# Performance work log

Measured on AMD Instinct MI355X. Metric: run time of the kernel, lower is better.

The kernel has to match this reference:

```python
import jax, jax.numpy as jnp
import numpy as np
from jax import lax

B, C, H, W = 8, 128, 128, 128
HEADS = 16
HEAD_C = C // HEADS  # 8
SLOPE = 0.2
EPS = 1e-12


def _conv(x, w, b, padding, groups=1):
    # x: [B,C,H,W], w: [O,I/groups,kh,kw]
    y = lax.conv_general_dilated(
        x, w, window_strides=(1, 1), padding=padding,
        dimension_numbers=("NCHW", "OIHW", "NCHW"),
        feature_group_count=groups)
    return y + b[None, :, None, None]


def _conv_block(x, conv1_w, conv1_b, conv2_w, conv2_b, dw_w, dw_b, sc_w, sc_b):
    h = _conv(x, conv1_w, conv1_b, ((1, 1), (1, 1)))            # 3x3, zero pad
    h = jnp.where(h >= 0, h, SLOPE * h)                          # LeakyReLU
    h = _conv(h, conv2_w, conv2_b, ((0, 0), (0, 0)))             # 1x1
    hp = jnp.pad(h, ((0, 0), (0, 0), (1, 1), (1, 1)), mode="reflect")
    h = _conv(hp, dw_w, dw_b, ((0, 0), (0, 0)), groups=C)        # depthwise 3x3, reflect pad
    h = jnp.where(h >= 0, h, SLOPE * h)
    sc = _conv(x, sc_w, sc_b, ((0, 0), (0, 0)))                  # 1x1 shortcut
    return h + sc


def setup_inputs() -> dict:
    key = jax.random.key(0)
    ks = jax.random.split(key, 10)
    s = 0.05
    return {
        "x1": jax.random.normal(ks[0], (B, C, H, W), jnp.float32),
        "x2": jax.random.normal(ks[1], (B, C, H, W), jnp.float32),
        "temperature": jnp.ones((HEADS, 1, 1), jnp.float32),
        "conv1_w": jax.random.normal(ks[2], (C, C, 3, 3), jnp.float32) * s,
        "conv1_b": jnp.zeros((C,), jnp.float32),
        "conv2_w": jax.random.normal(ks[3], (C, C, 1, 1), jnp.float32) * s,
        "conv2_b": jnp.zeros((C,), jnp.float32),
        "dw_w": jax.random.normal(ks[4], (C, 1, 3, 3), jnp.float32) * s,
        "dw_b": jnp.zeros((C,), jnp.float32),
        "sc_w": jax.random.normal(ks[5], (C, C, 1, 1), jnp.float32) * s,
        "sc_b": jnp.zeros((C,), jnp.float32),
    }


def reference(x1, x2, temperature, conv1_w, conv1_b, conv2_w, conv2_b,
              dw_w, dw_b, sc_w, sc_b):
    b, c, h, w = x2.shape
    # b (head c) h w -> b head c (h w)
    qk = x1.reshape(b, HEADS, HEAD_C, h * w)
    v = x2.reshape(b, HEADS, HEAD_C, h * w)
    # L2-normalize over spatial dim (F.normalize, eps=1e-12)
    norm = jnp.sqrt(jnp.sum(qk * qk, axis=-1, keepdims=True))
    qn = qk / jnp.maximum(norm, EPS)
    # channel attention: [b, head, c, c]
    attn = jnp.einsum("bhcn,bhdn->bhcd", qn, qn) * temperature
    attn = jax.nn.softmax(attn, axis=-1)
    out = jnp.einsum("bhcd,bhdn->bhcn", attn, v)
    out = out.reshape(b, c, h, w)
    out = _conv_block(out, conv1_w, conv1_b, conv2_w, conv2_b,
                      dw_w, dw_b, sc_w, sc_b)
    return out + x1
```

## Files before the change

kernel.cpp:

```cpp
#include <hip/hip_runtime.h>
#include <hip/hip_bf16.h>

typedef __attribute__((ext_vector_type(8))) short short8;
typedef __attribute__((ext_vector_type(4))) float f32x4;

#define NB 8
#define NC 128
#define NHW 128
#define NSP (NHW*NHW)
#define SLOPE 0.2f
#define EPSN 1e-12f

static __device__ __forceinline__ unsigned short f2bf(float f) {
    __hip_bfloat16 h = __float2bfloat16(f);
    return *reinterpret_cast<unsigned short*>(&h);
}
static __device__ __forceinline__ float bf2f(__hip_bfloat16 h) {
    return __bfloat162float(h);
}

__global__ void prep_wb1(const float* __restrict__ w, __hip_bfloat16* __restrict__ wb) {
    int idx = blockIdx.x * 256 + threadIdx.x;
    if (idx >= 128 * 128 * 9) return;
    int kw = idx % 3; int t = idx / 3;
    int kh = t % 3;   t /= 3;
    int i  = t % 128; int o = t / 128;
    int tap = kh * 3 + kw;
    int half = i >> 6, icc = (i >> 5) & 1, lk = (i >> 3) & 3, j = i & 7;
    int wn = o >> 6, c = (o >> 4) & 3, l15 = o & 15;
    int lane = lk * 16 + l15;
    size_t chunk = (size_t)tap * 32 + half * 16 + wn * 8 + icc * 4 + c;
    wb[chunk * 512 + lane * 8 + j] = __float2bfloat16(w[idx]);
}

__global__ void prep_w1x1(const float* __restrict__ w, __hip_bfloat16* __restrict__ wb) {
    int idx = blockIdx.x * 256 + threadIdx.x;
    if (idx >= 128 * 128) return;
    int i = idx & 127, o = idx >> 7;
    int kk = i >> 5, lk = (i >> 3) & 3, j = i & 7;
    int wn = o >> 6, c = (o >> 4) & 3, l15 = o & 15;
    int lane = lk * 16 + l15;
    size_t chunk = ((size_t)(wn * 4 + kk) * 4 + c);
    wb[chunk * 512 + lane * 8 + j] = __float2bfloat16(w[idx]);
}

__global__ __launch_bounds__(256) void gram_part(const float* __restrict__ x1,
                                                 float* __restrict__ Gp) {
    int bh = blockIdx.x & 127;
    int q  = blockIdx.x >> 7;
    const float* base = x1 + (size_t)bh * 8 * NSP + q * 4096;
    float acc[8][8];
#pragma unroll
    for (int c = 0; c < 8; c++)
#pragma unroll
        for (int d = 0; d < 8; d++) acc[c][d] = 0.f;

    for (int n = threadIdx.x; n < 4096; n += 256) {
        float v[8];
#pragma unroll
        for (int c = 0; c < 8; c++) v[c] = base[c * NSP + n];
#pragma unroll
        for (int c = 0; c < 8; c++)
#pragma unroll
            for (int d = 0; d < 8; d++)
                acc[c][d] = fmaf(v[c], v[d], acc[c][d]);
    }
#pragma unroll
    for (int c = 0; c < 8; c++)
#pragma unroll
        for (int d = 0; d < 8; d++)
            for (int off = 32; off > 0; off >>= 1)
                acc[c][d] += __shfl_down(acc[c][d], off);

    __shared__ float red[4][64];
    int wv = threadIdx.x >> 6;
    if ((threadIdx.x & 63) == 0) {
#pragma unroll
        for (int c = 0; c < 8; c++)
#pragma unroll
            for (int d = 0; d < 8; d++) red[wv][c * 8 + d] = acc[c][d];
    }
    __syncthreads();
    if (threadIdx.x < 64)
        Gp[(size_t)(q * 128 + bh) * 64 + threadIdx.x] =
            red[0][threadIdx.x] + red[1][threadIdx.x] + red[2][threadIdx.x] + red[3][threadIdx.x];
}

__global__ void gram_reduce(const float* __restrict__ Gp, float* __restrict__ G) {
    int bh = blockIdx.x;
    int t = threadIdx.x;
    float s = 0.f;
#pragma unroll
    for (int q = 0; q < 4; q++) s += Gp[(size_t)(q * 128 + bh) * 64 + t];
    G[bh * 64 + t] = s;
}

__global__ void softmax_kernel(const float* __restrict__ G, const float* __restrict__ temp,
                               float* __restrict__ attn) {
    int bh = blockIdx.x; int h = bh & 15;
    int t = threadIdx.x;
    int c = t >> 3, d = t & 7;
    const float* g = G + bh * 64;
    float nc = fmaxf(sqrtf(g[c * 8 + c]), EPSN);
    float nd = fmaxf(sqrtf(g[d * 8 + d]), EPSN);
    float a = g[t] / (nc * nd) * temp[h];
    float m = a;
#pragma unroll
    for (int off = 4; off > 0; off >>= 1) m = fmaxf(m, __shfl_xor(m, off));
    float e = __expf(a - m);
    float s = e;
#pragma unroll
    for (int off = 4; off > 0; off >>= 1) s += __shfl_xor(s, off);
    attn[bh * 64 + t] = e / s;
}

__global__ __launch_bounds__(256) void av_v2(const float* __restrict__ x2,
                                             const float* __restrict__ attn,
                                             __hip_bfloat16* __restrict__ yt) {
    int b  = blockIdx.x >> 8;
    int p0 = (blockIdx.x & 255) << 6;
    __shared__ float vt[128][65];
    __shared__ float at[16][65];
    for (int idx = threadIdx.x; idx < 1024; idx += 256)
        at[idx >> 6][idx & 63] = attn[(size_t)b * 1024 + idx];
    for (int idx = threadIdx.x; idx < 8192; idx += 256) {
        int row = idx >> 6, col = idx & 63;
        vt[row][col] = x2[(size_t)(b * 128 + row) * NSP + p0 + col];
    }
    __syncthreads();
    for (int idx = threadIdx.x; idx < 1024; idx += 256) {
        int cq = idx & 15;
        int p  = idx >> 4;
        float vv[8];
#pragma unroll
        for (int d = 0; d < 8; d++) vv[d] = vt[cq * 8 + d][p];
        unsigned int pk[4];
#pragma unroll
        for (int c = 0; c < 8; c += 2) {
            float s0 = 0.f, s1 = 0.f;
#pragma unroll
            for (int d = 0; d < 8; d++) {
                s0 = fmaf(at[cq][c * 8 + d], vv[d], s0);
                s1 = fmaf(at[cq][(c + 1) * 8 + d], vv[d], s1);
            }
            pk[c >> 1] = (unsigned int)f2bf(s0) | ((unsigned int)f2bf(s1) << 16);
        }
        uint4 st; st.x = pk[0]; st.y = pk[1]; st.z = pk[2]; st.w = pk[3];
        *reinterpret_cast<uint4*>(yt + ((size_t)b * NSP + p0 + p) * 128 + cq * 8) = st;
    }
}

__global__ __launch_bounds__(256, 4) void fused_conv(const __hip_bfloat16* __restrict__ yt,
                                                     const __hip_bfloat16* __restrict__ wb1,
                                                     const __hip_bfloat16* __restrict__ wb2,
                                                     const __hip_bfloat16* __restrict__ wbsc,
                                                     const float* __restrict__ b1,
                                                     const float* __restrict__ b2,
                                                     const float* __restrict__ bsc,
                                                     const float* __restrict__ x1,
                                                     __hip_bfloat16* __restrict__ h2,
                                                     float* __restrict__ out) {
    __shared__ uint4 smem[1584];
    char* smem_raw = (char*)smem;
    int bid = blockIdx.x;
    int swz = (bid & 7) * 256 + (bid >> 3);
    int b = swz >> 8;
    int rh = swz & 255;
    int h = rh >> 1;
    int p0 = (rh & 1) * 64;
    int tid = threadIdx.x;
    int lane = tid & 63;
    int wid = tid >> 6;
    int wm = wid >> 1, wn = wid & 1;
    int l15 = lane & 15;
    int lk = lane >> 4;

    const short8* wf1  = reinterpret_cast<const short8*>(wb1);
    const short8* wf2  = reinterpret_cast<const short8*>(wb2);
    const short8* wfsc = reinterpret_cast<const short8*>(wbsc);

    f32x4 acc[2][4];
#pragma unroll
    for (int a = 0; a < 2; a++)
#pragma unroll
        for (int c = 0; c < 4; c++) acc[a][c] = (f32x4){0.f, 0.f, 0.f, 0.f};

#pragma unroll
    for (int half = 0; half < 2; ++half) {
        __syncthreads();
        for (int idx = tid; idx < 1584; idx += 256) {
            int g = idx & 7;
            int colr = idx >> 3;
            int col = colr % 66;
            int r = colr / 66;
            int hh = h + r - 1;
            int w = p0 + col - 1;
            uint4 v = make_uint4(0u, 0u, 0u, 0u);
            if ((unsigned)hh < 128u && (unsigned)w < 128u)
                v = *reinterpret_cast<const uint4*>(
                    yt + (((size_t)(b * 128 + hh)) * 128 + w) * 128 + half * 64 + g * 8);
            smem[(r * 66 + col) * 8 + (g ^ (col & 7))] = v;
        }
        __syncthreads();

        int cgrp = half * 16 + wn * 8;
        const short8* wp0 = wf1 + (size_t)cgrp * 64 + lane;
        short8 cb0 = wp0[0], cb1 = wp0[64], cb2 = wp0[128], cb3 = wp0[192];

#pragma unroll
        for (int gi = 0; gi < 18; ++gi) {
            int tap = gi >> 1, icc = gi & 1;
            int kh = tap / 3, kw = tap - kh * 3;
            short8 nb0, nb1, nb2, nb3;
            if (gi < 17) {
                int gin = gi + 1;
                const short8* wpn = wf1 +
                    (size_t)(((gin >> 1) * 32) + cgrp + (gin & 1) * 4) * 64 + lane;
                nb0 = wpn[0]; nb1 = wpn[64]; nb2 = wpn[128]; nb3 = wpn[192];
            }
            short8 afr[2];
#pragma unroll
            for (int a = 0; a < 2; ++a) {
                int col = (wm * 2 + a) * 16 + l15 + kw;
                int g = icc * 4 + lk;
                afr[a] = *reinterpret_cast<const short8*>(
                    &smem[(kh * 66 + col) * 8 + (g ^ (col & 7))]);
            }
            __builtin_amdgcn_s_setprio(1);
#pragma unroll
            for (int a = 0; a < 2; ++a) {
                acc[a][0] = __builtin_amdgcn_mfma_f32_16x16x32_bf16(afr[a], cb0, acc[a][0], 0, 0, 0);
                acc[a][1] = __builtin_amdgcn_mfma_f32_16x16x32_bf16(afr[a], cb1, acc[a][1], 0, 0, 0);
                acc[a][2] = __builtin_amdgcn_mfma_f32_16x16x32_bf16(afr[a], cb2, acc[a][2], 0, 0, 0);
                acc[a][3] = __builtin_amdgcn_mfma_f32_16x16x32_bf16(afr[a], cb3, acc[a][3], 0, 0, 0);
            }
            __builtin_amdgcn_s_setprio(0);
            cb0 = nb0; cb1 = nb1; cb2 = nb2; cb3 = nb3;
        }
    }

    __syncthreads();
#pragma unroll
    for (int c = 0; c < 4; ++c) {
        int o = wn * 64 + c * 16 + l15;
        float bv = b1[o];
        int go = o >> 3, ob = (o & 7) << 1;
#pragma unroll
        for (int a = 0; a < 2; ++a) {
            int pb = (wm * 2 + a) * 16 + lk * 4;
#pragma unroll
            for (int j = 0; j < 4; ++j) {
                int p = pb + j;
                float v = acc[a][c][j] + bv;
                v = v >= 0.f ? v : SLOPE * v;
                *reinterpret_cast<__hip_bfloat16*>(
                    smem_raw + p * 256 + (((go ^ (p & 15)) << 4) | ob)) = __float2bfloat16(v);
            }
        }
    }
    __syncthreads();

#pragma unroll
    for (int a = 0; a < 2; a++)
#pragma unroll
        for (int c = 0; c < 4; c++) acc[a][c] = (f32x4){0.f, 0.f, 0.f, 0.f};
#pragma unroll
    for (int kk = 0; kk < 4; ++kk) {
        short8 bfr[4];
#pragma unroll
        for (int c = 0; c < 4; ++c)
            bfr[c] = wf2[((size_t)(wn * 4 + kk) * 4 + c) * 64 + lane];
        short8 afr[2];
        int g = kk * 4 + lk;
#pragma unroll
        for (int a = 0; a < 2; ++a) {
            int p = (wm * 2 + a) * 16 + l15;
            afr[a] = *reinterpret_cast<const short8*>(smem_raw + p * 256 + ((g ^ (p & 15)) << 4));
        }
        __builtin_amdgcn_s_setprio(1);
#pragma unroll
        for (int a = 0; a < 2; ++a)
#pragma unroll
            for (int c = 0; c < 4; ++c)
                acc[a][c] = __builtin_amdgcn_mfma_f32_16x16x32_bf16(afr[a], bfr[c], acc[a][c], 0, 0, 0);
        __builtin_amdgcn_s_setprio(0);
    }
#pragma unroll
    for (int c = 0; c < 4; ++c) {
        int o = wn * 64 + c * 16 + l15;
        float bv = b2[o];
        size_t obase = ((size_t)(b * 128 + o) * 128 + h) * 128 + p0;
#pragma unroll
        for (int a = 0; a < 2; ++a) {
            int w0 = (wm * 2 + a) * 16 + lk * 4;
            uint2 st;
            st.x = (unsigned int)f2bf(acc[a][c][0] + bv) | ((unsigned int)f2bf(acc[a][c][1] + bv) << 16);
            st.y = (unsigned int)f2bf(acc[a][c][2] + bv) | ((unsigned int)f2bf(acc[a][c][3] + bv) << 16);
            *reinterpret_cast<uint2*>(h2 + obase + w0) = st;
        }
    }

    __syncthreads();
    for (int idx = tid; idx < 1024; idx += 256) {
        int p = idx >> 4, g = idx & 15;
        uint4 v = *reinterpret_cast<const uint4*>(
            yt + ((size_t)(b * NSP + h * 128 + p0 + p)) * 128 + g * 8);
        *reinterpret_cast<uint4*>(smem_raw + p * 256 + ((g ^ (p & 15)) << 4)) = v;
    }
    __syncthreads();

#pragma unroll
    for (int a = 0; a < 2; a++)
#pragma unroll
        for (int c = 0; c < 4; c++) acc[a][c] = (f32x4){0.f, 0.f, 0.f, 0.f};
#pragma unroll
    for (int kk = 0; kk < 4; ++kk) {
        short8 bfr[4];
#pragma unroll
        for (int c = 0; c < 4; ++c)
            bfr[c] = wfsc[((size_t)(wn * 4 + kk) * 4 + c) * 64 + lane];
        short8 afr[2];
        int g = kk * 4 + lk;
#pragma unroll
        for (int a = 0; a < 2; ++a) {
            int p = (wm * 2 + a) * 16 + l15;
            afr[a] = *reinterpret_cast<const short8*>(smem_raw + p * 256 + ((g ^ (p & 15)) << 4));
        }
        __builtin_amdgcn_s_setprio(1);
#pragma unroll
        for (int a = 0; a < 2; ++a)
#pragma unroll
            for (int c = 0; c < 4; ++c)
                acc[a][c] = __builtin_amdgcn_mfma_f32_16x16x32_bf16(afr[a], bfr[c], acc[a][c], 0, 0, 0);
        __builtin_amdgcn_s_setprio(0);
    }
#pragma unroll
    for (int c = 0; c < 4; ++c) {
        int o = wn * 64 + c * 16 + l15;
        float bv = bsc[o];
        size_t obase = ((size_t)(b * 128 + o) * 128 + h) * 128 + p0;
#pragma unroll
        for (int a = 0; a < 2; ++a) {
            int w0 = (wm * 2 + a) * 16 + lk * 4;
            float4 xv = *reinterpret_cast<const float4*>(x1 + obase + w0);
            float4 st;
            st.x = acc[a][c][0] + bv + xv.x;
            st.y = acc[a][c][1] + bv + xv.y;
            st.z = acc[a][c][2] + bv + xv.z;
            st.w = acc[a][c][3] + bv + xv.w;
            *reinterpret_cast<float4*>(out + obase + w0) = st;
        }
    }
}

__global__ __launch_bounds__(256) void dw_v2(const __hip_bfloat16* __restrict__ h2,
                                             const float* __restrict__ dww,
                                             const float* __restrict__ dwb,
                                             float* __restrict__ out) {
    int bid = blockIdx.x;
    int swz = (bid & 7) * 1024 + (bid >> 3);
    size_t tidx = (size_t)swz * 256 + threadIdx.x;
    int w0 = (int)((tidx & 15) << 3);
    int hh = (int)((tidx >> 4) & 127);
    int bc = (int)(tidx >> 11);
    int c  = bc & 127;
    const __hip_bfloat16* src = h2 + ((size_t)bc << 14);
    float wg[9];
#pragma unroll
    for (int k = 0; k < 9; ++k) wg[k] = dww[c * 9 + k];
    float bv = dwb[c];
    float a8[8];
#pragma unroll
    for (int j = 0; j < 8; ++j) a8[j] = bv;
#pragma unroll
    for (int kh = 0; kh < 3; ++kh) {
        int ih = hh + kh - 1;
        ih = ih < 0 ? 1 : (ih > 127 ? 126 : ih);
        const __hip_bfloat16* row = src + ih * 128;
        short8 mid = *reinterpret_cast<const short8*>(row + w0);
        float v[10];
        v[0] = bf2f(row[w0 == 0 ? 1 : w0 - 1]);
#pragma unroll
        for (int j = 0; j < 8; ++j)
            v[j + 1] = __uint_as_float((unsigned int)(unsigned short)mid[j] << 16);
        v[9] = bf2f(row[w0 == 120 ? 126 : w0 + 8]);
#pragma unroll
        for (int kw = 0; kw < 3; ++kw)
#pragma unroll
            for (int j = 0; j < 8; ++j)
                a8[j] = fmaf(v[j + kw], wg[kh * 3 + kw], a8[j]);
    }
    size_t ob = ((size_t)bc << 14) + hh * 128 + w0;
    float4 o0 = *reinterpret_cast<const float4*>(out + ob);
    float4 o1 = *reinterpret_cast<const float4*>(out + ob + 4);
#pragma unroll
    for (int j = 0; j < 8; ++j) a8[j] = a8[j] >= 0.f ? a8[j] : SLOPE * a8[j];
    o0.x += a8[0]; o0.y += a8[1]; o0.z += a8[2]; o0.w += a8[3];
    o1.x += a8[4]; o1.y += a8[5]; o1.z += a8[6]; o1.w += a8[7];
    *reinterpret_cast<float4*>(out + ob) = o0;
    *reinterpret_cast<float4*>(out + ob + 4) = o1;
}

extern "C" void kernel_launch(void* const* d_in, const int* in_sizes, int n_in,
                              void* d_out, int out_size, void* d_ws, size_t ws_size,
                              hipStream_t stream) {
    const float* x1   = (const float*)d_in[0];
    const float* x2   = (const float*)d_in[1];
    const float* temp = (const float*)d_in[2];
    const float* c1w  = (const float*)d_in[3];
    const float* c1b  = (const float*)d_in[4];
    const float* c2w  = (const float*)d_in[5];
    const float* c2b  = (const float*)d_in[6];
    const float* dww  = (const float*)d_in[7];
    const float* dwb  = (const float*)d_in[8];
    const float* scw  = (const float*)d_in[9];
    const float* scb  = (const float*)d_in[10];
    float* out = (float*)d_out;
    char* ws = (char*)d_ws;

    float*          G    = (float*)(ws);
    float*          attn = (float*)(ws + (32 << 10));
    float*          Gp   = (float*)(ws + (64 << 10));
    __hip_bfloat16* wb1  = (__hip_bfloat16*)(ws + (192 << 10));
    __hip_bfloat16* wb2  = (__hip_bfloat16*)(ws + (480 << 10));
    __hip_bfloat16* wbsc = (__hip_bfloat16*)(ws + (512 << 10));
    __hip_bfloat16* yt   = (__hip_bfloat16*)(ws + ((size_t)1 << 20));
    __hip_bfloat16* h2b  = (__hip_bfloat16*)(ws + ((size_t)34 << 20));

    prep_wb1<<<576, 256, 0, stream>>>(c1w, wb1);
    prep_w1x1<<<64, 256, 0, stream>>>(c2w, wb2);
    prep_w1x1<<<64, 256, 0, stream>>>(scw, wbsc);

    gram_part<<<512, 256, 0, stream>>>(x1, Gp);
    gram_reduce<<<128, 64, 0, stream>>>(Gp, G);
    softmax_kernel<<<128, 64, 0, stream>>>(G, temp, attn);
    av_v2<<<2048, 256, 0, stream>>>(x2, attn, yt);

    fused_conv<<<2048, 256, 0, stream>>>(yt, wb1, wb2, wbsc, c1b, c2b, scb, x1, h2b, out);
    dw_v2<<<8192, 256, 0, stream>>>(h2b, dww, dwb, out);
}
```

Measured before the change: 162.4 us.

## Use zero-padded activation layout and two-stage weight prefetch in conv

```diff
diff --git a/kernel.cpp b/kernel.cpp
--- a/kernel.cpp
+++ b/kernel.cpp
@@ -10,6 +10,7 @@
 #define NSP (NHW*NHW)
 #define SLOPE 0.2f
 #define EPSN 1e-12f
+#define PADW 130
 
 static __device__ __forceinline__ unsigned short f2bf(float f) {
     __hip_bfloat16 h = __float2bfloat16(f);
@@ -44,6 +45,21 @@
     wb[chunk * 512 + lane * 8 + j] = __float2bfloat16(w[idx]);
 }
 
+__global__ void pad_zero(__hip_bfloat16* __restrict__ yt2) {
+    int t = blockIdx.x * 256 + threadIdx.x;
+    if (t >= 8 * 516) return;
+    int b = t / 516, s = t % 516;
+    int row, col;
+    if (s < 130)      { row = 0;           col = s; }
+    else if (s < 260) { row = 129;         col = s - 130; }
+    else if (s < 388) { row = s - 260 + 1; col = 0; }
+    else              { row = s - 388 + 1; col = 129; }
+    uint4* dst = reinterpret_cast<uint4*>(yt2 + ((size_t)(b * PADW + row) * PADW + col) * 128);
+    uint4 z = make_uint4(0u, 0u, 0u, 0u);
+#pragma unroll
+    for (int i = 0; i < 16; ++i) dst[i] = z;
+}
+
 __global__ __launch_bounds__(256) void gram_part(const float* __restrict__ x1,
                                                  float* __restrict__ Gp) {
     int bh = blockIdx.x & 127;
@@ -114,9 +130,9 @@
     attn[bh * 64 + t] = e / s;
 }
 
-__global__ __launch_bounds__(256) void av_v2(const float* __restrict__ x2,
+__global__ __launch_bounds__(256) void av_v3(const float* __restrict__ x2,
                                              const float* __restrict__ attn,
-                                             __hip_bfloat16* __restrict__ yt) {
+                                             __hip_bfloat16* __restrict__ yt2) {
     int b  = blockIdx.x >> 8;
     int p0 = (blockIdx.x & 255) << 6;
     __shared__ float vt[128][65];
@@ -146,11 +162,16 @@
             pk[c >> 1] = (unsigned int)f2bf(s0) | ((unsigned int)f2bf(s1) << 16);
         }
         uint4 st; st.x = pk[0]; st.y = pk[1]; st.z = pk[2]; st.w = pk[3];
-        *reinterpret_cast<uint4*>(yt + ((size_t)b * NSP + p0 + p) * 128 + cq * 8) = st;
-    }
-}
-
-__global__ __launch_bounds__(256, 4) void fused_conv(const __hip_bfloat16* __restrict__ yt,
+        int n = p0 + p;
+        int hh = n >> 7, wc = n & 127;
+        *reinterpret_cast<uint4*>(
+            yt2 + ((size_t)(b * PADW + hh + 1) * PADW + wc + 1) * 128 + cq * 8) = st;
+    }
+}
+
+#define BPTR(s) (wf1 + ((size_t)(((((s) % 18) >> 1) * 32) + ((s) / 18) * 16 + wn * 8 + ((s) & 1) * 4)) * 64 + lane)
+
+__global__ __launch_bounds__(256, 4) void fused_conv(const __hip_bfloat16* __restrict__ yt2,
                                                      const __hip_bfloat16* __restrict__ wb1,
                                                      const __hip_bfloat16* __restrict__ wb2,
                                                      const __hip_bfloat16* __restrict__ wbsc,
@@ -185,6 +206,11 @@
 #pragma unroll
         for (int c = 0; c < 4; c++) acc[a][c] = (f32x4){0.f, 0.f, 0.f, 0.f};
 
+    const short8* wpi = BPTR(0);
+    short8 bA0 = wpi[0], bA1 = wpi[64], bA2 = wpi[128], bA3 = wpi[192];
+    wpi = BPTR(1);
+    short8 bB0 = wpi[0], bB1 = wpi[64], bB2 = wpi[128], bB3 = wpi[192];
+
 #pragma unroll
     for (int half = 0; half < 2; ++half) {
         __syncthreads();
@@ -193,49 +219,69 @@
             int colr = idx >> 3;
             int col = colr % 66;
             int r = colr / 66;
-            int hh = h + r - 1;
-            int w = p0 + col - 1;
-            uint4 v = make_uint4(0u, 0u, 0u, 0u);
-            if ((unsigned)hh < 128u && (unsigned)w < 128u)
-                v = *reinterpret_cast<const uint4*>(
-                    yt + (((size_t)(b * 128 + hh)) * 128 + w) * 128 + half * 64 + g * 8);
+            uint4 v = *reinterpret_cast<const uint4*>(
+                yt2 + ((size_t)(b * PADW + h + r) * PADW + (p0 + col)) * 128 + half * 64 + g * 8);
             smem[(r * 66 + col) * 8 + (g ^ (col & 7))] = v;
         }
         __syncthreads();
 
-        int cgrp = half * 16 + wn * 8;
-        const short8* wp0 = wf1 + (size_t)cgrp * 64 + lane;
-        short8 cb0 = wp0[0], cb1 = wp0[64], cb2 = wp0[128], cb3 = wp0[192];
-
-#pragma unroll
-        for (int gi = 0; gi < 18; ++gi) {
-            int tap = gi >> 1, icc = gi & 1;
-            int kh = tap / 3, kw = tap - kh * 3;
-            short8 nb0, nb1, nb2, nb3;
-            if (gi < 17) {
-                int gin = gi + 1;
-                const short8* wpn = wf1 +
-                    (size_t)(((gin >> 1) * 32) + cgrp + (gin & 1) * 4) * 64 + lane;
-                nb0 = wpn[0]; nb1 = wpn[64]; nb2 = wpn[128]; nb3 = wpn[192];
+#pragma unroll
+        for (int gp = 0; gp < 9; ++gp) {
+            const int kh = gp / 3, kw = gp - kh * 3;
+            {
+                const int s = half * 18 + gp * 2;
+                short8 n0, n1, n2, n3;
+                const bool more = (s + 2 < 36);
+                if (more) {
+                    const short8* w2 = BPTR(s + 2);
+                    n0 = w2[0]; n1 = w2[64]; n2 = w2[128]; n3 = w2[192];
+                }
+                short8 afr[2];
+#pragma unroll
+                for (int a = 0; a < 2; ++a) {
+                    int col = (wm * 2 + a) * 16 + l15 + kw;
+                    int g = lk;
+                    afr[a] = *reinterpret_cast<const short8*>(
+                        &smem[(kh * 66 + col) * 8 + (g ^ (col & 7))]);
+                }
+                __builtin_amdgcn_s_setprio(1);
+#pragma unroll
+                for (int a = 0; a < 2; ++a) {
+                    acc[a][0] = __builtin_amdgcn_mfma_f32_16x16x32_bf16(afr[a], bA0, acc[a][0], 0, 0, 0);
+                    acc[a][1] = __builtin_amdgcn_mfma_f32_16x16x32_bf16(afr[a], bA1, acc[a][1], 0, 0, 0);
+                    acc[a][2] = __builtin_amdgcn_mfma_f32_16x16x32_bf16(afr[a], bA2, acc[a][2], 0, 0, 0);
+                    acc[a][3] = __builtin_amdgcn_mfma_f32_16x16x32_bf16(afr[a], bA3, acc[a][3], 0, 0, 0);
+                }
+                __builtin_amdgcn_s_setprio(0);
+                if (more) { bA0 = n0; bA1 = n1; bA2 = n2; bA3 = n3; }
             }
-            short8 afr[2];
-#pragma unroll
-            for (int a = 0; a < 2; ++a) {
-                int col = (wm * 2 + a) * 16 + l15 + kw;
-                int g = icc * 4 + lk;
-                afr[a] = *reinterpret_cast<const short8*>(
-                    &smem[(kh * 66 + col) * 8 + (g ^ (col & 7))]);
+            {
+                const int s = half * 18 + gp * 2 + 1;
+                short8 n0, n1, n2, n3;
+                const bool more = (s + 2 < 36);
+                if (more) {
+                    const short8* w2 = BPTR(s + 2);
+                    n0 = w2[0]; n1 = w2[64]; n2 = w2[128]; n3 = w2[192];
+                }
+                short8 afr[2];
+#pragma unroll
+                for (int a = 0; a < 2; ++a) {
+                    int col = (wm * 2 + a) * 16 + l15 + kw;
+                    int g = 4 + lk;
+                    afr[a] = *reinterpret_cast<const short8*>(
+                        &smem[(kh * 66 + col) * 8 + (g ^ (col & 7))]);
+                }
+                __builtin_amdgcn_s_setprio(1);
+#pragma unroll
+                for (int a = 0; a < 2; ++a) {
+                    acc[a][0] = __builtin_amdgcn_mfma_f32_16x16x32_bf16(afr[a], bB0, acc[a][0], 0, 0, 0);
+                    acc[a][1] = __builtin_amdgcn_mfma_f32_16x16x32_bf16(afr[a], bB1, acc[a][1], 0, 0, 0);
+                    acc[a][2] = __builtin_amdgcn_mfma_f32_16x16x32_bf16(afr[a], bB2, acc[a][2], 0, 0, 0);
+                    acc[a][3] = __builtin_amdgcn_mfma_f32_16x16x32_bf16(afr[a], bB3, acc[a][3], 0, 0, 0);
+                }
+                __builtin_amdgcn_s_setprio(0);
+                if (more) { bB0 = n0; bB1 = n1; bB2 = n2; bB3 = n3; }
             }
-            __builtin_amdgcn_s_setprio(1);
-#pragma unroll
-            for (int a = 0; a < 2; ++a) {
-                acc[a][0] = __builtin_amdgcn_mfma_f32_16x16x32_bf16(afr[a], cb0, acc[a][0], 0, 0, 0);
-                acc[a][1] = __builtin_amdgcn_mfma_f32_16x16x32_bf16(afr[a], cb1, acc[a][1], 0, 0, 0);
-                acc[a][2] = __builtin_amdgcn_mfma_f32_16x16x32_bf16(afr[a], cb2, acc[a][2], 0, 0, 0);
-                acc[a][3] = __builtin_amdgcn_mfma_f32_16x16x32_bf16(afr[a], cb3, acc[a][3], 0, 0, 0);
-            }
-            __builtin_amdgcn_s_setprio(0);
-            cb0 = nb0; cb1 = nb1; cb2 = nb2; cb3 = nb3;
         }
     }
 
@@ -304,7 +350,7 @@
     for (int idx = tid; idx < 1024; idx += 256) {
         int p = idx >> 4, g = idx & 15;
         uint4 v = *reinterpret_cast<const uint4*>(
-            yt + ((size_t)(b * NSP + h * 128 + p0 + p)) * 128 + g * 8);
+            yt2 + ((size_t)(b * PADW + h + 1) * PADW + (p0 + 1 + p)) * 128 + g * 8);
         *reinterpret_cast<uint4*>(smem_raw + p * 256 + ((g ^ (p & 15)) << 4)) = v;
     }
     __syncthreads();
@@ -424,18 +470,19 @@
     __hip_bfloat16* wb1  = (__hip_bfloat16*)(ws + (192 << 10));
     __hip_bfloat16* wb2  = (__hip_bfloat16*)(ws + (480 << 10));
     __hip_bfloat16* wbsc = (__hip_bfloat16*)(ws + (512 << 10));
-    __hip_bfloat16* yt   = (__hip_bfloat16*)(ws + ((size_t)1 << 20));
-    __hip_bfloat16* h2b  = (__hip_bfloat16*)(ws + ((size_t)34 << 20));
+    __hip_bfloat16* yt2  = (__hip_bfloat16*)(ws + ((size_t)1 << 20));
+    __hip_bfloat16* h2b  = (__hip_bfloat16*)(ws + ((size_t)36 << 20));
 
     prep_wb1<<<576, 256, 0, stream>>>(c1w, wb1);
     prep_w1x1<<<64, 256, 0, stream>>>(c2w, wb2);
     prep_w1x1<<<64, 256, 0, stream>>>(scw, wbsc);
+    pad_zero<<<17, 256, 0, stream>>>(yt2);
 
     gram_part<<<512, 256, 0, stream>>>(x1, Gp);
     gram_reduce<<<128, 64, 0, stream>>>(Gp, G);
     softmax_kernel<<<128, 64, 0, stream>>>(G, temp, attn);
-    av_v2<<<2048, 256, 0, stream>>>(x2, attn, yt);
-
-    fused_conv<<<2048, 256, 0, stream>>>(yt, wb1, wb2, wbsc, c1b, c2b, scb, x1, h2b, out);
+    av_v3<<<2048, 256, 0, stream>>>(x2, attn, yt2);
+
+    fused_conv<<<2048, 256, 0, stream>>>(yt2, wb1, wb2, wbsc, c1b, c2b, scb, x1, h2b, out);
     dw_v2<<<8192, 256, 0, stream>>>(h2b, dww, dwb, out);
 }
```

After: 167.7 us. +3.3%, slower.
